# Optimization experiments

Measured on AMD Instinct MI355X. Metric: run time of the kernel, lower is better.

## Reference

```python
import jax, jax.numpy as jnp
import numpy as np
from jax import lax

B, Z = 64, 64
H_IMG, W_IMG = 480, 640
BASE_C, Z_C = 64, 32


def setup_inputs() -> dict:
    key = jax.random.key(0)
    k1, k2, k3, k4, k5, k6 = jax.random.split(key, 6)
    hist_BZ2 = jax.random.uniform(k1, (B, Z, 2), dtype=jnp.float32) * 2.0
    mask_BZ = jax.random.uniform(k2, (B, Z)) > 0.1
    # 8x8 zone grid tiling the HxW image with 60x80 tiles (sy, sx, ey, ex)
    zi = jnp.arange(Z)
    row, col = zi // 8, zi % 8
    bh, bw = H_IMG // 8, W_IMG // 8
    fr = jnp.stack([row * bh, col * bw, (row + 1) * bh, (col + 1) * bw], axis=-1).astype(jnp.int32)
    fr_BZ4 = jnp.broadcast_to(fr[None], (B, Z, 4))
    w1 = jax.random.normal(k3, (BASE_C, 2, 1, 1), dtype=jnp.float32) * 0.1
    b1 = jax.random.normal(k4, (BASE_C,), dtype=jnp.float32) * 0.01
    w2 = jax.random.normal(k5, (Z_C, BASE_C, 3, 3), dtype=jnp.float32) * 0.05
    b2 = jax.random.normal(k6, (Z_C,), dtype=jnp.float32) * 0.01
    return {"hist_BZ2": hist_BZ2, "mask_BZ": mask_BZ, "fr_BZ4": fr_BZ4,
            "H": H_IMG, "W": W_IMG, "w1": w1, "b1": b1, "w2": w2, "b2": b2}


def _build_dense(tof_mean, tof_var, mask_BZ, fr_BZ4, H, W):
    # scanned over the Z zones (Z=64 small, fixed).
    b = tof_mean.shape[0]
    ys = jnp.arange(H)[:, None]  # [H,1]
    xs = jnp.arange(W)[None, :]  # [1,W]

    def step(dense, per_zone):
        m, v, mk, box = per_zone  # m,v,mk: [B]; box: [B,4] int
        sy = jnp.maximum(box[:, 0], 0)
        sx = jnp.maximum(box[:, 1], 0)
        ey = jnp.minimum(box[:, 2], H)
        ex = jnp.minimum(box[:, 3], W)
        cover = ((ys[None] >= sy[:, None, None]) & (ys[None] < ey[:, None, None]) &
                 (xs[None] >= sx[:, None, None]) & (xs[None] < ex[:, None, None]) &
                 mk[:, None, None])  # [B,H,W]
        vals = jnp.stack([m, v], axis=1)[:, :, None, None]  # [B,2,1,1]
        dense = jnp.where(cover[:, None], vals, dense)
        return dense, None

    dense0 = jnp.zeros((b, 2, H, W), dtype=tof_mean.dtype)
    zone_inputs = (tof_mean.T, tof_var.T, mask_BZ.T, jnp.swapaxes(fr_BZ4, 0, 1))
    dense, _ = lax.scan(step, dense0, zone_inputs)
    return dense


def _conv(x, w, b, pad):
    y = lax.conv_general_dilated(x, w, (1, 1), pad,
                                 dimension_numbers=("NCHW", "OIHW", "NCHW"))
    return y + b[None, :, None, None]


def reference(hist_BZ2, mask_BZ, fr_BZ4, H, W, w1, b1, w2, b2):
    mk = mask_BZ.astype(hist_BZ2.dtype)
    tof_mean = hist_BZ2[..., 0] * mk
    tof_var = hist_BZ2[..., 1] * mk
    dense = _build_dense(tof_mean, tof_var, mask_BZ, fr_BZ4, H, W)
    # F.interpolate(mode='area') to (8,8): exact block-average since H,W % 8 == 0
    b = dense.shape[0]
    tof_map = dense.reshape(b, 2, 8, H // 8, 8, W // 8).mean(axis=(3, 5))
    x = jnp.log1p(jnp.maximum(tof_map, 0))
    x = _conv(x, w1, b1, "VALID")          # 1x1 conv
    x = jax.nn.silu(x)
    x = _conv(x, w2, b2, [(1, 1), (1, 1)])  # 3x3 conv, padding 1
    return x
```

## Files before the change

kernel.cpp:

```cpp
#include <hip/hip_runtime.h>
#include <math.h>


__global__ __launch_bounds__(256) void tof_fused(
    const float* __restrict__ hist,
    const int*   __restrict__ mask,
    const float* __restrict__ w1,
    const float* __restrict__ b1,
    const float* __restrict__ w2,
    const float* __restrict__ b2,
    float* __restrict__ out)
{
    const int b = blockIdx.x;
    const int oc_base = blockIdx.y * 8;
    const int t = threadIdx.x;

    __shared__ float xs[2][64];
    __shared__ float x1s[64][10][12];

    float* x1f = &x1s[0][0][0];
    for (int k = t; k < 64 * 10 * 12; k += 256) x1f[k] = 0.f;

    if (t < 64) {
        const int z = t;
        const float mk = (mask[b * 64 + z] != 0) ? 1.f : 0.f;
        const float m = hist[(b * 64 + z) * 2 + 0] * mk;
        const float v = hist[(b * 64 + z) * 2 + 1] * mk;
        xs[0][z] = log1pf(fmaxf(m, 0.f));
        xs[1][z] = log1pf(fmaxf(v, 0.f));
    }
    __syncthreads();

    #pragma unroll
    for (int k = 0; k < 16; ++k) {
        const int idx = t + k * 256;
        const int o   = idx >> 6;
        const int pos = idx & 63;
        const int r = pos >> 3, c = pos & 7;
        float v = fmaf(w1[o * 2 + 0], xs[0][pos],
                  fmaf(w1[o * 2 + 1], xs[1][pos], b1[o]));
        v = v / (1.f + expf(-v));
        x1s[o][r + 1][c + 1] = v;
    }
    __syncthreads();

    const int o_local = t >> 5;
    const int o = oc_base + o_local;
    const int r = (t >> 2) & 7;
    const int c0 = (t & 3) * 2;

    float acc0 = b2[o], acc1 = b2[o];
    const float* __restrict__ w2o = w2 + (size_t)o * 64 * 9;

    #pragma unroll 4
    for (int i = 0; i < 64; ++i) {
        const float* __restrict__ w = w2o + i * 9;
        const float w00 = w[0], w01 = w[1], w02 = w[2];
        const float w10 = w[3], w11 = w[4], w12 = w[5];
        const float w20 = w[6], w21 = w[7], w22 = w[8];
        const float* row0 = &x1s[i][r + 0][c0];
        const float* row1 = &x1s[i][r + 1][c0];
        const float* row2 = &x1s[i][r + 2][c0];
        const float a0 = row0[0], a1 = row0[1], a2 = row0[2], a3 = row0[3];
        acc0 = fmaf(w00, a0, fmaf(w01, a1, fmaf(w02, a2, acc0)));
        acc1 = fmaf(w00, a1, fmaf(w01, a2, fmaf(w02, a3, acc1)));
        const float d0 = row1[0], d1 = row1[1], d2 = row1[2], d3 = row1[3];
        acc0 = fmaf(w10, d0, fmaf(w11, d1, fmaf(w12, d2, acc0)));
        acc1 = fmaf(w10, d1, fmaf(w11, d2, fmaf(w12, d3, acc1)));
        const float e0 = row2[0], e1 = row2[1], e2 = row2[2], e3 = row2[3];
        acc0 = fmaf(w20, e0, fmaf(w21, e1, fmaf(w22, e2, acc0)));
        acc1 = fmaf(w20, e1, fmaf(w21, e2, fmaf(w22, e3, acc1)));
    }

    const int base = ((b * 32 + o) * 8 + r) * 8 + c0;
    out[base + 0] = acc0;
    out[base + 1] = acc1;
}

extern "C" void kernel_launch(void* const* d_in, const int* in_sizes, int n_in,
                              void* d_out, int out_size, void* d_ws, size_t ws_size,
                              hipStream_t stream) {
    const float* hist = (const float*)d_in[0];
    const int*   mask = (const int*)d_in[1];
    const float* w1 = (const float*)d_in[5];
    const float* b1 = (const float*)d_in[6];
    const float* w2 = (const float*)d_in[7];
    const float* b2 = (const float*)d_in[8];
    float* out = (float*)d_out;

    tof_fused<<<dim3(64, 4), dim3(256), 0, stream>>>(hist, mask, w1, b1, w2, b2, out);
}
```

Baseline: 78.67 us.

## Stage conv weights in LDS, one output per thread, double block count

```diff
diff --git a/kernel.cpp b/kernel.cpp
--- a/kernel.cpp
+++ b/kernel.cpp
@@ -12,14 +12,22 @@
     float* __restrict__ out)
 {
     const int b = blockIdx.x;
-    const int oc_base = blockIdx.y * 8;
+    const int oc_base = blockIdx.y * 4;
     const int t = threadIdx.x;
 
     __shared__ float xs[2][64];
     __shared__ float x1s[64][10][12];
+    __shared__ float w2s[4 * 64 * 9];
 
     float* x1f = &x1s[0][0][0];
-    for (int k = t; k < 64 * 10 * 12; k += 256) x1f[k] = 0.f;
+    #pragma unroll
+    for (int k = 0; k < 30; ++k) x1f[t + k * 256] = 0.f;
+
+    {
+        const float* __restrict__ src = w2 + (size_t)oc_base * 576;
+        #pragma unroll
+        for (int k = 0; k < 9; ++k) w2s[t + k * 256] = src[t + k * 256];
+    }
 
     if (t < 64) {
         const int z = t;
@@ -44,37 +52,26 @@
     }
     __syncthreads();
 
-    const int o_local = t >> 5;
-    const int o = oc_base + o_local;
-    const int r = (t >> 2) & 7;
-    const int c0 = (t & 3) * 2;
+    const int oc_local = t >> 6;
+    const int o = oc_base + oc_local;
+    const int r = (t >> 3) & 7;
+    const int c = t & 7;
 
-    float acc0 = b2[o], acc1 = b2[o];
-    const float* __restrict__ w2o = w2 + (size_t)o * 64 * 9;
+    float acc = b2[o];
+    const float* __restrict__ wbase = &w2s[oc_local * 576];
 
     #pragma unroll 4
     for (int i = 0; i < 64; ++i) {
-        const float* __restrict__ w = w2o + i * 9;
-        const float w00 = w[0], w01 = w[1], w02 = w[2];
-        const float w10 = w[3], w11 = w[4], w12 = w[5];
-        const float w20 = w[6], w21 = w[7], w22 = w[8];
-        const float* row0 = &x1s[i][r + 0][c0];
-        const float* row1 = &x1s[i][r + 1][c0];
-        const float* row2 = &x1s[i][r + 2][c0];
-        const float a0 = row0[0], a1 = row0[1], a2 = row0[2], a3 = row0[3];
-        acc0 = fmaf(w00, a0, fmaf(w01, a1, fmaf(w02, a2, acc0)));
-        acc1 = fmaf(w00, a1, fmaf(w01, a2, fmaf(w02, a3, acc1)));
-        const float d0 = row1[0], d1 = row1[1], d2 = row1[2], d3 = row1[3];
-        acc0 = fmaf(w10, d0, fmaf(w11, d1, fmaf(w12, d2, acc0)));
-        acc1 = fmaf(w10, d1, fmaf(w11, d2, fmaf(w12, d3, acc1)));
-        const float e0 = row2[0], e1 = row2[1], e2 = row2[2], e3 = row2[3];
-        acc0 = fmaf(w20, e0, fmaf(w21, e1, fmaf(w22, e2, acc0)));
-        acc1 = fmaf(w20, e1, fmaf(w21, e2, fmaf(w22, e3, acc1)));
+        const float* __restrict__ w = wbase + i * 9;
+        const float* row0 = &x1s[i][r + 0][c];
+        const float* row1 = &x1s[i][r + 1][c];
+        const float* row2 = &x1s[i][r + 2][c];
+        acc = fmaf(w[0], row0[0], fmaf(w[1], row0[1], fmaf(w[2], row0[2], acc)));
+        acc = fmaf(w[3], row1[0], fmaf(w[4], row1[1], fmaf(w[5], row1[2], acc)));
+        acc = fmaf(w[6], row2[0], fmaf(w[7], row2[1], fmaf(w[8], row2[2], acc)));
     }
 
-    const int base = ((b * 32 + o) * 8 + r) * 8 + c0;
-    out[base + 0] = acc0;
-    out[base + 1] = acc1;
+    out[((b * 32 + o) * 8 + r) * 8 + c] = acc;
 }
 
 extern "C" void kernel_launch(void* const* d_in, const int* in_sizes, int n_in,
@@ -88,5 +85,5 @@
     const float* b2 = (const float*)d_in[8];
     float* out = (float*)d_out;
 
-    tof_fused<<<dim3(64, 4), dim3(256), 0, stream>>>(hist, mask, w1, b1, w2, b2, out);
+    tof_fused<<<dim3(64, 8), dim3(256), 0, stream>>>(hist, mask, w1, b1, w2, b2, out);
 }
```

Measured after the change: 82.54 us. 4.9% more time.
